# Kernel optimization log

Hardware: AMD Instinct MI355X
Metric: run time of the kernel (lower is better)

Reference implementation:

```python
import jax, jax.numpy as jnp
import numpy as np

B, S, D, H = 2, 2048, 1024, 16
HD = D // H  # 64


def rotate_half(x):
    x1, x2 = x[..., : x.shape[-1] // 2], x[..., x.shape[-1] // 2 :]
    return jnp.concatenate((-x2, x1), axis=-1)


def setup_inputs() -> dict:
    key = jax.random.key(0)
    ks = jax.random.split(key, 8)
    return {
        "hidden_states": jax.random.normal(ks[0], (B, S, D), jnp.float32),
        "attention_bias": jax.random.normal(ks[1], (B, 1, S, S), jnp.float32),
        "cos": jax.random.uniform(ks[2], (1, S, 1, HD), jnp.float32),
        "sin": jax.random.uniform(ks[3], (1, S, 1, HD), jnp.float32),
        "Wqkv": jax.random.normal(ks[4], (D, 3 * D), jnp.float32) * (D ** -0.5),
        "bqkv": jnp.zeros((3 * D,), jnp.float32),
        "Wo": jax.random.normal(ks[5], (D, D), jnp.float32) * (D ** -0.5),
        "bo": jnp.zeros((D,), jnp.float32),
    }


def reference(hidden_states, attention_bias, cos, sin, Wqkv, bqkv, Wo, bo):
    # packed QKV projection: [B,S,D] -> [B,S,3D]
    qkv = hidden_states @ Wqkv + bqkv
    q, k, v = jnp.split(qkv, 3, axis=-1)
    # reshape to [B,S,H,HD]
    q = q.reshape(B, S, H, HD)
    k = k.reshape(B, S, H, HD)
    v = v.reshape(B, S, H, HD)
    # rotary position embedding
    q = q * cos + rotate_half(q) * sin
    k = k * cos + rotate_half(k) * sin
    # scaled dot-product attention with additive bias
    scores = jnp.einsum("bqhd,bkhd->bhqk", q, k) / jnp.sqrt(jnp.float32(HD))
    scores = scores + attention_bias
    probs = jax.nn.softmax(scores, axis=-1)
    ctx = jnp.einsum("bhqk,bkhd->bqhd", probs, v)  # [B,S,H,HD]
    ctx = ctx.reshape(B, S, D)
    return ctx @ Wo + bo
```

## Files before the change

kernel.cpp:

```cpp
#include <hip/hip_runtime.h>
#include <stdint.h>

typedef unsigned short u16;
typedef __attribute__((ext_vector_type(8))) short short8;
typedef __attribute__((ext_vector_type(4))) float f32x4;

#define DI __device__ __forceinline__

constexpr int S_LEN = 2048;
constexpr float LOG2E = 1.44269504088896f;
constexpr float SC = 0.125f * 1.44269504088896f;

DI float bf2f(u16 u) { union { uint32_t i; float f; } v; v.i = ((uint32_t)u) << 16; return v.f; }
DI u16 f2bf(float f) {
  union { float f; uint32_t i; } v; v.f = f;
  return (u16)((v.i + 0x7FFFu + ((v.i >> 16) & 1u)) >> 16);
}
DI uint32_t cvtpk(float lo, float hi) {
  uint32_t r;
  asm("v_cvt_pk_bf16_f32 %0, %1, %2" : "=v"(r) : "v"(lo), "v"(hi));
  return r;
}
DI float exp2r(float x) {
  float r;
  asm("v_exp_f32 %0, %1" : "=v"(r) : "v"(x));
  return r;
}

DI void cp16(const void* g, void* l) {
  auto gp = reinterpret_cast<const __attribute__((address_space(1))) uint32_t*>(
      reinterpret_cast<uintptr_t>(g));
  auto lp = reinterpret_cast<__attribute__((address_space(3))) uint32_t*>(
      reinterpret_cast<uintptr_t>(l));
  __builtin_amdgcn_global_load_lds(gp, lp, 16, 0, 0);
}

DI f32x4 mfma16(short8 a, short8 b, f32x4 c) {
  return __builtin_amdgcn_mfma_f32_16x16x32_bf16(a, b, c, 0, 0, 0);
}

DI int permk(int rl) {
  return ((rl >> 5) & 1) * 32 + ((rl >> 2) & 3) * 8 + ((rl >> 4) & 1) * 4 + (rl & 3);
}

__global__ __launch_bounds__(256) void k_prep(const float* __restrict__ hs,
                                              u16* __restrict__ h_bf,
                                              const float* __restrict__ bias,
                                              u16* __restrict__ biasbf,
                                              const float* __restrict__ Wqkv,
                                              u16* __restrict__ wqkvT,
                                              const float* __restrict__ Wo,
                                              u16* __restrict__ woT) {
  int bid = blockIdx.x;
  int tid = threadIdx.x;
  if (bid < 4096) {
    int i = bid * 256 + tid;
    float4 v = ((const float4*)hs)[i];
    ushort4 o = { f2bf(v.x), f2bf(v.y), f2bf(v.z), f2bf(v.w) };
    ((ushort4*)h_bf)[i] = o;
    return;
  }
  if (bid < 12288) {
    int i = (bid - 4096) * 256 + tid;
    float4 v = ((const float4*)bias)[i];
    ushort4 o = { f2bf(v.x * LOG2E), f2bf(v.y * LOG2E),
                  f2bf(v.z * LOG2E), f2bf(v.w * LOG2E) };
    ((ushort4*)biasbf)[i] = o;
    return;
  }
  __shared__ float t[32][33];
  int tt = bid - 12288;
  int bx = tt & 127, by = tt >> 7;
  const float* in;
  u16* out;
  int C;
  if (bx < 96) { in = Wqkv; out = wqkvT; C = 3072; }
  else         { bx -= 96; in = Wo; out = woT; C = 1024; }
  constexpr int R = 1024;
  int tx = tid & 31, ty = tid >> 5;
  int c0 = bx * 32, r0 = by * 32;
#pragma unroll
  for (int k = 0; k < 4; k++)
    t[ty + 8 * k][tx] = in[(size_t)(r0 + ty + 8 * k) * C + c0 + tx];
  __syncthreads();
#pragma unroll
  for (int k = 0; k < 4; k++)
    out[(size_t)(c0 + ty + 8 * k) * R + r0 + tx] = f2bf(t[tx][ty + 8 * k]);
}

template <int BM, int STORE_F32, int QKV>
__global__ __launch_bounds__(256) void k_gemm(const u16* __restrict__ A,
                                              const u16* __restrict__ Bt,
                                              const float* __restrict__ bias,
                                              void* __restrict__ Cout,
                                              u16* __restrict__ vtg,
                                              const float* __restrict__ cosb,
                                              const float* __restrict__ sinb,
                                              int N, int K, int nbx) {
  constexpr int NJ = (BM == 128) ? 4 : 2;
  __shared__ u16 Al[BM * 64];
  __shared__ u16 Bl[128 * 64];
  int nwg = gridDim.x;
  int per = nwg >> 3;
  int id = blockIdx.x;
  int sid = (id & 7) * per + (id >> 3);
  int bx = sid % nbx, by = sid / nbx;
  int row0 = by * BM, col0 = bx * 128;
  int tid = threadIdx.x;
  int lane = tid & 63, wave = tid >> 6;
  int lg = lane >> 4, lc = lane & 15;
  int wroff = (BM == 128) ? (wave >> 1) * 64 : 0;
  int wcoff = (BM == 128) ? (wave & 1) * 64 : wave * 32;
  int srow = tid >> 3, sseg = tid & 7;
  int sw = (sseg ^ (srow & 7)) * 8;
  const u16* ga = A + (size_t)(row0 + srow) * K + sw;
  const u16* gb = Bt + (size_t)(col0 + srow) * K + sw;
  f32x4 acc[4][NJ] = {};
  for (int ko = 0; ko < K; ko += 64) {
#pragma unroll
    for (int p = 0; p < BM / 32; p++)
      cp16(ga + (size_t)p * 32 * K + ko, Al + tid * 8 + p * 2048);
#pragma unroll
    for (int p = 0; p < 4; p++)
      cp16(gb + (size_t)p * 32 * K + ko, Bl + tid * 8 + p * 2048);
    __syncthreads();
#pragma unroll
    for (int kk = 0; kk < 2; kk++) {
      short8 af[4], bf[NJ];
#pragma unroll
      for (int i = 0; i < 4; i++) {
        int row = wroff + i * 16 + lc;
        af[i] = *(const short8*)&Al[row * 64 + (((kk * 4 + lg) ^ (row & 7)) * 8)];
      }
#pragma unroll
      for (int j = 0; j < NJ; j++) {
        int row = wcoff + j * 16 + lc;
        bf[j] = *(const short8*)&Bl[row * 64 + (((kk * 4 + lg) ^ (row & 7)) * 8)];
      }
#pragma unroll
      for (int i = 0; i < 4; i++)
#pragma unroll
        for (int j = 0; j < NJ; j++) acc[i][j] = mfma16(af[i], bf[j], acc[i][j]);
    }
    __syncthreads();
  }
  int cbase = col0 + wcoff + lc;
  float bv[NJ];
#pragma unroll
  for (int j = 0; j < NJ; j++) bv[j] = bias[cbase + j * 16];

  if constexpr (QKV) {
    if (col0 >= 2048) {
#pragma unroll
      for (int i = 0; i < 4; i++) {
        int r = row0 + wroff + i * 16 + lg * 4;
        int bq = r >> 11, s0 = r & 2047;
#pragma unroll
        for (int j = 0; j < NJ; j++) {
          int c = cbase + j * 16 - 2048;
          int h = c >> 6, d = c & 63;
          ushort4 o4 = { f2bf(acc[i][j][0] + bv[j]), f2bf(acc[i][j][1] + bv[j]),
                         f2bf(acc[i][j][2] + bv[j]), f2bf(acc[i][j][3] + bv[j]) };
          *(ushort4*)&vtg[(size_t)(bq * 16 + h) * 131072 + (size_t)d * 2048 + s0] = o4;
        }
      }
      return;
    }
  }
#pragma unroll
  for (int i = 0; i < 4; i++) {
    int r = row0 + wroff + i * 16 + lg * 4;
#pragma unroll
    for (int q = 0; q < 4; q++) {
      float v[NJ];
#pragma unroll
      for (int j = 0; j < NJ; j++) v[j] = acc[i][j][q] + bv[j];
      if constexpr (QKV) {
        int s = (r + q) & 2047;
        const float* cb = cosb + s * 64 + lc;
        const float* sb = sinb + s * 64 + lc;
#pragma unroll
        for (int jp = 0; jp < 2; jp++) {
          float cl = cb[jp * 16], sl = sb[jp * 16];
          float ch = cb[jp * 16 + 32], sh = sb[jp * 16 + 32];
          float x1 = v[jp], x2 = v[jp + 2];
          v[jp] = x1 * cl - x2 * sl;
          v[jp + 2] = x2 * ch + x1 * sh;
        }
      }
#pragma unroll
      for (int j = 0; j < NJ; j++) {
        if constexpr (STORE_F32)
          ((float*)Cout)[(size_t)(r + q) * N + cbase + j * 16] = v[j];
        else
          ((u16*)Cout)[(size_t)(r + q) * N + cbase + j * 16] = f2bf(v[j]);
      }
    }
  }
}

DI float sm_pa(const f32x4 st[4], const short8* bc, short8 pa[2]) {
  float acc = 0.f;
  uint32_t w[4][2];
#pragma unroll
  for (int j = 0; j < 4; j++) {
    int base = (j & 1) * 4;
    float b0 = bf2f((u16)(j < 2 ? bc[0][base + 0] : bc[1][base + 0]));
    float b1 = bf2f((u16)(j < 2 ? bc[0][base + 1] : bc[1][base + 1]));
    float b2 = bf2f((u16)(j < 2 ? bc[0][base + 2] : bc[1][base + 2]));
    float b3 = bf2f((u16)(j < 2 ? bc[0][base + 3] : bc[1][base + 3]));
    float e0 = exp2r(st[j][0] * SC + b0);
    float e1 = exp2r(st[j][1] * SC + b1);
    float e2 = exp2r(st[j][2] * SC + b2);
    float e3 = exp2r(st[j][3] * SC + b3);
    acc += (e0 + e1) + (e2 + e3);
    w[j][0] = cvtpk(e0, e1);
    w[j][1] = cvtpk(e2, e3);
  }
  union { short8 s; uint32_t u[4]; } p0, p1;
  p0.u[0] = w[0][0]; p0.u[1] = w[0][1]; p0.u[2] = w[1][0]; p0.u[3] = w[1][1];
  p1.u[0] = w[2][0]; p1.u[1] = w[2][1]; p1.u[2] = w[3][0]; p1.u[3] = w[3][1];
  pa[0] = p0.s;
  pa[1] = p1.s;
  return acc;
}

DI void attn_store(u16* __restrict__ ctx, const f32x4 o[4], float lsumT,
                   size_t rowbase, int hcol, int lg, int lc) {
  float rinv[4];
#pragma unroll
  for (int r = 0; r < 4; r++) rinv[r] = 1.0f / __shfl(lsumT, lg * 4 + r);
#pragma unroll
  for (int j = 0; j < 4; j++)
#pragma unroll
    for (int r = 0; r < 4; r++)
      ctx[(rowbase + lg * 4 + r) * 1024 + hcol + j * 16 + lc] =
          f2bf(o[j][r] * rinv[r]);
}

__global__ __launch_bounds__(256, 2) void k_attn(const u16* __restrict__ qkv,
                                                 const u16* __restrict__ biasl2,
                                                 const u16* __restrict__ vtg,
                                                 u16* __restrict__ ctx) {
  __shared__ u16 Kl[2][4096];
  __shared__ u16 Vl[2][4096];
  constexpr int nkt = 32;
  int id = blockIdx.x;
  int idx = id >> 3;
  int bh = (id & 7) * 4 + (idx & 3);
  int qt = idx >> 2;
  int b = bh >> 4, h = bh & 15;
  int tid = threadIdx.x, lane = tid & 63, wave = tid >> 6;
  int lg = lane >> 4, lc = lane & 15;
  int q0 = qt * 128 + wave * 32;

  const u16* qb = qkv + (size_t)(b * S_LEN + q0 + lc) * 3072 + h * 64 + lg * 8;
  short8 qf[2][2];
#pragma unroll
  for (int s = 0; s < 2; s++) {
    qf[s][0] = *(const short8*)(qb + (size_t)s * 16 * 3072);
    qf[s][1] = *(const short8*)(qb + (size_t)s * 16 * 3072 + 32);
  }

  int srow = tid >> 3, sseg = tid & 7;
  const u16* kst[2];
  const u16* vst[2];
#pragma unroll
  for (int p = 0; p < 2; p++) {
    int rl = srow + 32 * p;
    int sw = (sseg ^ (rl & 7)) * 8;
    kst[p] = qkv + (size_t)(b * S_LEN + permk(rl)) * 3072 + 1024 + h * 64 + sw;
    vst[p] = vtg + (size_t)bh * 64 * 2048 + (size_t)rl * 2048 + sw;
  }

  const u16* bp0 = biasl2 + ((size_t)b * S_LEN + q0 + lc) * 2048 + lg * 8;
  const u16* bp1 = bp0 + (size_t)16 * 2048;

  f32x4 o0[4] = {}, o1[4] = {};
  float lsum0 = 0.f, lsum1 = 0.f;

#pragma unroll
  for (int p = 0; p < 2; p++) {
    cp16(kst[p], (u16*)&Kl[0][0] + p * 2048 + tid * 8);
    cp16(vst[p], (u16*)&Vl[0][0] + p * 2048 + tid * 8);
    kst[p] += (size_t)64 * 3072;
    vst[p] += 64;
  }
  short8 bA[4], bB[4];
  bA[0] = *(const short8*)bp0;
  bA[1] = *(const short8*)(bp0 + 32);
  bA[2] = *(const short8*)bp1;
  bA[3] = *(const short8*)(bp1 + 32);
  bp0 += 64;
  bp1 += 64;
  __syncthreads();

  auto tile = [&](int kt, int cur, const short8* bc, short8* bn) {
    if (kt < nkt - 1) {
#pragma unroll
      for (int p = 0; p < 2; p++) {
        cp16(kst[p], (u16*)&Kl[cur ^ 1][0] + p * 2048 + tid * 8);
        cp16(vst[p], (u16*)&Vl[cur ^ 1][0] + p * 2048 + tid * 8);
        kst[p] += (size_t)64 * 3072;
        vst[p] += 64;
      }
      bn[0] = *(const short8*)bp0;
      bn[1] = *(const short8*)(bp0 + 32);
      bn[2] = *(const short8*)bp1;
      bn[3] = *(const short8*)(bp1 + 32);
      bp0 += 64;
      bp1 += 64;
    }
    f32x4 st0[4] = {}, st1[4] = {};
    __builtin_amdgcn_s_setprio(1);
#pragma unroll
    for (int kk = 0; kk < 2; kk++) {
      short8 kf[4];
#pragma unroll
      for (int j = 0; j < 4; j++) {
        int row = j * 16 + lc;
        kf[j] = *(const short8*)&Kl[cur][row * 64 + (((kk * 4 + lg) ^ (row & 7)) * 8)];
      }
#pragma unroll
      for (int j = 0; j < 4; j++) {
        st0[j] = mfma16(kf[j], qf[0][kk], st0[j]);
        st1[j] = mfma16(kf[j], qf[1][kk], st1[j]);
      }
    }
    __builtin_amdgcn_s_setprio(0);
    short8 pa0[2], pa1[2];
    lsum0 += sm_pa(st0, bc, pa0);
    lsum1 += sm_pa(st1, bc + 2, pa1);
    __builtin_amdgcn_s_setprio(1);
#pragma unroll
    for (int kk = 0; kk < 2; kk++) {
      short8 vf[4];
#pragma unroll
      for (int j = 0; j < 4; j++) {
        int row = j * 16 + lc;
        vf[j] = *(const short8*)&Vl[cur][row * 64 + (((kk * 4 + lg) ^ (row & 7)) * 8)];
      }
#pragma unroll
      for (int j = 0; j < 4; j++) {
        o0[j] = mfma16(pa0[kk], vf[j], o0[j]);
        o1[j] = mfma16(pa1[kk], vf[j], o1[j]);
      }
    }
    __builtin_amdgcn_s_setprio(0);
    __syncthreads();
  };

  for (int kt = 0; kt < nkt; kt += 2) {
    tile(kt, 0, bA, bB);
    tile(kt + 1, 1, bB, bA);
  }

  float t0 = lsum0;
  t0 += __shfl_xor(t0, 16);
  t0 += __shfl_xor(t0, 32);
  float t1 = lsum1;
  t1 += __shfl_xor(t1, 16);
  t1 += __shfl_xor(t1, 32);
  size_t rowbase = (size_t)b * S_LEN + q0;
  attn_store(ctx, o0, t0, rowbase, h * 64, lg, lc);
  attn_store(ctx, o1, t1, rowbase + 16, h * 64, lg, lc);
}

extern "C" void kernel_launch(void* const* d_in, const int* in_sizes, int n_in,
                              void* d_out, int out_size, void* d_ws, size_t ws_size,
                              hipStream_t stream) {
  (void)in_sizes; (void)n_in; (void)out_size; (void)ws_size;
  const float* hs   = (const float*)d_in[0];
  const float* bias = (const float*)d_in[1];
  const float* cosb = (const float*)d_in[2];
  const float* sinb = (const float*)d_in[3];
  const float* Wqkv = (const float*)d_in[4];
  const float* bqkv = (const float*)d_in[5];
  const float* Wo   = (const float*)d_in[6];
  const float* bo   = (const float*)d_in[7];
  float* out = (float*)d_out;
  char* ws = (char*)d_ws;
  u16* h_bf   = (u16*)(ws + 0);
  u16* wqkvT  = (u16*)(ws + 8388608);
  u16* woT    = (u16*)(ws + 14680064);
  u16* biasbf = (u16*)(ws + 16777216);
  u16* qkv    = (u16*)(ws + 33554432);
  u16* vtg    = (u16*)(ws + 58720256);
  u16* ctxb   = (u16*)(ws + 67108864);

  k_prep<<<16384, 256, 0, stream>>>(hs, h_bf, bias, biasbf, Wqkv, wqkvT, Wo, woT);
  k_gemm<128, 0, 1><<<768, 256, 0, stream>>>(h_bf, wqkvT, bqkv, qkv, vtg,
                                             cosb, sinb, 3072, 1024, 24);
  k_attn<<<512, 256, 0, stream>>>(qkv, biasbf, vtg, ctxb);
  k_gemm<64, 1, 0><<<512, 256, 0, stream>>>(ctxb, woT, bo, out, nullptr,
                                            nullptr, nullptr, 1024, 1024, 8);
}
```

Before: 140.3 us.

## Double KV tile size in attention kernel to 128 keys per iteration

```diff
diff --git a/kernel.cpp b/kernel.cpp
--- a/kernel.cpp
+++ b/kernel.cpp
@@ -39,8 +39,8 @@
   return __builtin_amdgcn_mfma_f32_16x16x32_bf16(a, b, c, 0, 0, 0);
 }
 
-DI int permk(int rl) {
-  return ((rl >> 5) & 1) * 32 + ((rl >> 2) & 3) * 8 + ((rl >> 4) & 1) * 4 + (rl & 3);
+DI int permk128(int rl) {
+  return ((rl >> 5) & 3) * 32 + ((rl >> 2) & 3) * 8 + ((rl >> 4) & 1) * 4 + (rl & 3);
 }
 
 __global__ __launch_bounds__(256) void k_prep(const float* __restrict__ hs,
@@ -199,16 +199,17 @@
   }
 }
 
-DI float sm_pa(const f32x4 st[4], const short8* bc, short8 pa[2]) {
+DI float sm_pa(const f32x4 st[8], const short8 bc[4], short8 pa[4]) {
   float acc = 0.f;
-  uint32_t w[4][2];
-#pragma unroll
-  for (int j = 0; j < 4; j++) {
+  uint32_t w[8][2];
+#pragma unroll
+  for (int j = 0; j < 8; j++) {
     int base = (j & 1) * 4;
-    float b0 = bf2f((u16)(j < 2 ? bc[0][base + 0] : bc[1][base + 0]));
-    float b1 = bf2f((u16)(j < 2 ? bc[0][base + 1] : bc[1][base + 1]));
-    float b2 = bf2f((u16)(j < 2 ? bc[0][base + 2] : bc[1][base + 2]));
-    float b3 = bf2f((u16)(j < 2 ? bc[0][base + 3] : bc[1][base + 3]));
+    short8 bb = bc[j >> 1];
+    float b0 = bf2f((u16)bb[base + 0]);
+    float b1 = bf2f((u16)bb[base + 1]);
+    float b2 = bf2f((u16)bb[base + 2]);
+    float b3 = bf2f((u16)bb[base + 3]);
     float e0 = exp2r(st[j][0] * SC + b0);
     float e1 = exp2r(st[j][1] * SC + b1);
     float e2 = exp2r(st[j][2] * SC + b2);
@@ -217,11 +218,15 @@
     w[j][0] = cvtpk(e0, e1);
     w[j][1] = cvtpk(e2, e3);
   }
-  union { short8 s; uint32_t u[4]; } p0, p1;
-  p0.u[0] = w[0][0]; p0.u[1] = w[0][1]; p0.u[2] = w[1][0]; p0.u[3] = w[1][1];
-  p1.u[0] = w[2][0]; p1.u[1] = w[2][1]; p1.u[2] = w[3][0]; p1.u[3] = w[3][1];
-  pa[0] = p0.s;
-  pa[1] = p1.s;
+#pragma unroll
+  for (int kk = 0; kk < 4; kk++) {
+    union { short8 s; uint32_t u[4]; } p;
+    p.u[0] = w[2 * kk][0];
+    p.u[1] = w[2 * kk][1];
+    p.u[2] = w[2 * kk + 1][0];
+    p.u[3] = w[2 * kk + 1][1];
+    pa[kk] = p.s;
+  }
   return acc;
 }
 
@@ -242,9 +247,9 @@
                                                  const u16* __restrict__ biasl2,
                                                  const u16* __restrict__ vtg,
                                                  u16* __restrict__ ctx) {
-  __shared__ u16 Kl[2][4096];
-  __shared__ u16 Vl[2][4096];
-  constexpr int nkt = 32;
+  __shared__ u16 Kl[2][8192];
+  __shared__ u16 Vl[2][8192];
+  constexpr int nkt = 16;
   int id = blockIdx.x;
   int idx = id >> 3;
   int bh = (id & 7) * 4 + (idx & 3);
@@ -263,15 +268,19 @@
   }
 
   int srow = tid >> 3, sseg = tid & 7;
-  const u16* kst[2];
-  const u16* vst[2];
-#pragma unroll
-  for (int p = 0; p < 2; p++) {
+  const u16* kst[4];
+#pragma unroll
+  for (int p = 0; p < 4; p++) {
     int rl = srow + 32 * p;
     int sw = (sseg ^ (rl & 7)) * 8;
-    kst[p] = qkv + (size_t)(b * S_LEN + permk(rl)) * 3072 + 1024 + h * 64 + sw;
-    vst[p] = vtg + (size_t)bh * 64 * 2048 + (size_t)rl * 2048 + sw;
-  }
+    kst[p] = qkv + (size_t)(b * S_LEN + permk128(rl)) * 3072 + 1024 + h * 64 + sw;
+  }
+  int vrow = tid >> 4, vseg = tid & 15;
+  int sw_v = (vseg ^ vrow) * 8;
+  const u16* vst[4];
+#pragma unroll
+  for (int c = 0; c < 4; c++)
+    vst[c] = vtg + (size_t)bh * 131072 + (size_t)(c * 16 + vrow) * 2048 + sw_v;
 
   const u16* bp0 = biasl2 + ((size_t)b * S_LEN + q0 + lc) * 2048 + lg * 8;
   const u16* bp1 = bp0 + (size_t)16 * 2048;
@@ -280,65 +289,68 @@
   float lsum0 = 0.f, lsum1 = 0.f;
 
 #pragma unroll
-  for (int p = 0; p < 2; p++) {
+  for (int p = 0; p < 4; p++) {
     cp16(kst[p], (u16*)&Kl[0][0] + p * 2048 + tid * 8);
     cp16(vst[p], (u16*)&Vl[0][0] + p * 2048 + tid * 8);
-    kst[p] += (size_t)64 * 3072;
-    vst[p] += 64;
-  }
-  short8 bA[4], bB[4];
-  bA[0] = *(const short8*)bp0;
-  bA[1] = *(const short8*)(bp0 + 32);
-  bA[2] = *(const short8*)bp1;
-  bA[3] = *(const short8*)(bp1 + 32);
-  bp0 += 64;
-  bp1 += 64;
+    kst[p] += (size_t)128 * 3072;
+    vst[p] += 128;
+  }
+  short8 bA0[4], bA1[4], bB0[4], bB1[4];
+#pragma unroll
+  for (int c = 0; c < 4; c++) {
+    bA0[c] = *(const short8*)(bp0 + c * 32);
+    bA1[c] = *(const short8*)(bp1 + c * 32);
+  }
+  bp0 += 128;
+  bp1 += 128;
   __syncthreads();
 
-  auto tile = [&](int kt, int cur, const short8* bc, short8* bn) {
+  auto tile = [&](int kt, int cur, const short8* bc0, const short8* bc1,
+                  short8* bn0, short8* bn1) {
     if (kt < nkt - 1) {
 #pragma unroll
-      for (int p = 0; p < 2; p++) {
+      for (int p = 0; p < 4; p++) {
         cp16(kst[p], (u16*)&Kl[cur ^ 1][0] + p * 2048 + tid * 8);
         cp16(vst[p], (u16*)&Vl[cur ^ 1][0] + p * 2048 + tid * 8);
-        kst[p] += (size_t)64 * 3072;
-        vst[p] += 64;
-      }
-      bn[0] = *(const short8*)bp0;
-      bn[1] = *(const short8*)(bp0 + 32);
-      bn[2] = *(const short8*)bp1;
-      bn[3] = *(const short8*)(bp1 + 32);
-      bp0 += 64;
-      bp1 += 64;
-    }
-    f32x4 st0[4] = {}, st1[4] = {};
+        kst[p] += (size_t)128 * 3072;
+        vst[p] += 128;
+      }
+#pragma unroll
+      for (int c = 0; c < 4; c++) {
+        bn0[c] = *(const short8*)(bp0 + c * 32);
+        bn1[c] = *(const short8*)(bp1 + c * 32);
+      }
+      bp0 += 128;
+      bp1 += 128;
+    }
+    f32x4 st0[8] = {}, st1[8] = {};
     __builtin_amdgcn_s_setprio(1);
 #pragma unroll
     for (int kk = 0; kk < 2; kk++) {
-      short8 kf[4];
-#pragma unroll
-      for (int j = 0; j < 4; j++) {
+      short8 kf[8];
+#pragma unroll
+      for (int j = 0; j < 8; j++) {
         int row = j * 16 + lc;
         kf[j] = *(const short8*)&Kl[cur][row * 64 + (((kk * 4 + lg) ^ (row & 7)) * 8)];
       }
 #pragma unroll
-      for (int j = 0; j < 4; j++) {
+      for (int j = 0; j < 8; j++) {
         st0[j] = mfma16(kf[j], qf[0][kk], st0[j]);
         st1[j] = mfma16(kf[j], qf[1][kk], st1[j]);
       }
     }
     __builtin_amdgcn_s_setprio(0);
-    short8 pa0[2], pa1[2];
-    lsum0 += sm_pa(st0, bc, pa0);
-    lsum1 += sm_pa(st1, bc + 2, pa1);
+    short8 pa0[4], pa1[4];
+    lsum0 += sm_pa(st0, bc0, pa0);
+    lsum1 += sm_pa(st1, bc1, pa1);
     __builtin_amdgcn_s_setprio(1);
 #pragma unroll
-    for (int kk = 0; kk < 2; kk++) {
+    for (int kk = 0; kk < 4; kk++) {
       short8 vf[4];
 #pragma unroll
       for (int j = 0; j < 4; j++) {
-        int row = j * 16 + lc;
-        vf[j] = *(const short8*)&Vl[cur][row * 64 + (((kk * 4 + lg) ^ (row & 7)) * 8)];
+        int d = j * 16 + lc;
+        vf[j] = *(const short8*)&Vl[cur][d * 128 + (((kk * 4 + lg) ^ (d & 15)) * 8)];
       }
 #pragma unroll
       for (int j = 0; j < 4; j++) {
@@ -351,8 +363,8 @@
   };
 
   for (int kt = 0; kt < nkt; kt += 2) {
-    tile(kt, 0, bA, bB);
-    tile(kt + 1, 1, bB, bA);
+    tile(kt, 0, bA0, bA1, bB0, bB1);
+    tile(kt + 1, 1, bB0, bB1, bA0, bA1);
   }
 
   float t0 = lsum0;
```

New measurement: 143.9 us. 1.03x slower.
